# Kernel optimization log

Hardware: AMD Instinct MI355X
Metric: run time of the kernel (lower is better)

The kernel has to match this reference:

```python
import jax, jax.numpy as jnp
import numpy as np

N_NODES = 50000
N_EDGES = 800000
D_FEAT = 64


def setup_inputs() -> dict:
    key = jax.random.key(0)
    k_x, k_e, k_w = jax.random.split(key, 3)
    x = jax.random.normal(k_x, (N_NODES, D_FEAT), dtype=jnp.float32)
    edge_index = jax.random.randint(k_e, (2, N_EDGES), 0, N_NODES, dtype=jnp.int64)
    # message MLP params (phi_Theta): single linear + ReLU
    W = jax.random.normal(k_w, (D_FEAT, D_FEAT), dtype=jnp.float32) / np.sqrt(D_FEAT)
    b = jnp.zeros((D_FEAT,), dtype=jnp.float32)
    return {"x": x, "edge_index": edge_index, "W": W, "b": b}


def reference(x, edge_index, W, b):
    # flow = source_to_target: messages flow from edge_index[0] (j) to edge_index[1] (i)
    src = edge_index[0]  # j: source nodes (gather)
    dst = edge_index[1]  # i: target nodes (scatter index)
    n_nodes = x.shape[0]
    # __collect__: index_select gather of source node features -> x_j [E, D]
    x_j = x[src]
    # message: per-edge MLP  phi(x_j) = relu(x_j W + b)
    msg = jax.nn.relu(jnp.einsum('ed,df->ef', x_j, W) + b)
    # aggregate: scatter-add into target nodes (aggr='add', dim_size = size_i)
    out = jax.ops.segment_sum(msg, dst, num_segments=n_nodes)
    # update: identity
    return out
```

## Files before the change

### kernel.cpp

```cpp
#include <hip/hip_runtime.h>
#include <hip/hip_bf16.h>

#define D 64
#define CAP 64
#define EUNROLL 4

__device__ __forceinline__ float bf2f(unsigned short u) {
    return __uint_as_float((unsigned int)u << 16);
}
__device__ __forceinline__ unsigned short f2bf(float f) {
    unsigned int u = __float_as_uint(f);
    unsigned int r = (u + 0x7fffu + ((u >> 16) & 1u)) >> 16;
    return (unsigned short)r;
}

__global__ __launch_bounds__(256) void node_mlp_kernel(
    const float* __restrict__ x, const float* __restrict__ W,
    const float* __restrict__ b, unsigned short* __restrict__ m,
    int* __restrict__ cnt, int n_nodes) {
    for (int i = blockIdx.x * blockDim.x + threadIdx.x; i < n_nodes;
         i += gridDim.x * blockDim.x) cnt[i] = 0;

    const int lane = threadIdx.x & 63;
    float w[D];
    #pragma unroll
    for (int k = 0; k < D; ++k) w[k] = W[k * D + lane];
    const float bias = b[lane];

    const int wave = (blockIdx.x * blockDim.x + threadIdx.x) >> 6;
    const int nwaves = (gridDim.x * blockDim.x) >> 6;

    for (int row = wave; row < n_nodes; row += nwaves) {
        const float4* xr = (const float4*)(x + (size_t)row * D);
        float acc = bias;
        #pragma unroll
        for (int kk = 0; kk < D / 4; ++kk) {
            float4 xv = xr[kk];
            acc = fmaf(xv.x, w[4 * kk + 0], acc);
            acc = fmaf(xv.y, w[4 * kk + 1], acc);
            acc = fmaf(xv.z, w[4 * kk + 2], acc);
            acc = fmaf(xv.w, w[4 * kk + 3], acc);
        }
        m[(size_t)row * D + lane] = f2bf(fmaxf(acc, 0.0f));
    }
}

__global__ __launch_bounds__(256) void append_kernel(
    const int* __restrict__ src, const int* __restrict__ dst,
    int* __restrict__ cnt, unsigned short* __restrict__ slots, int n_edges) {
    const int base = blockIdx.x * 256 * EUNROLL + threadIdx.x;
    int s[EUNROLL], d[EUNROLL], pos[EUNROLL];
    bool ok[EUNROLL];
    #pragma unroll
    for (int i = 0; i < EUNROLL; ++i) {
        int e = base + i * 256;
        ok[i] = (e < n_edges);
        s[i] = ok[i] ? src[e] : 0;
        d[i] = ok[i] ? dst[e] : 0;
    }
    #pragma unroll
    for (int i = 0; i < EUNROLL; ++i)
        pos[i] = ok[i] ? atomicAdd(&cnt[d[i]], 1) : CAP;
    #pragma unroll
    for (int i = 0; i < EUNROLL; ++i)
        if (ok[i] && pos[i] < CAP)
            slots[(size_t)d[i] * CAP + pos[i]] = (unsigned short)s[i];
}

__global__ __launch_bounds__(256) void gather_accum_kernel(
    const unsigned short* __restrict__ slots, const int* __restrict__ cnt,
    const unsigned short* __restrict__ m, float* __restrict__ out, int n_nodes) {
    int node = blockIdx.x * 4 + (threadIdx.x >> 6);
    if (node >= n_nodes) return;
    int lane = threadIdx.x & 63;

    int c = min(cnt[node], CAP);
    unsigned int idx = (lane < c) ? (unsigned int)slots[(size_t)node * CAP + lane] : 0u;

    float acc = 0.0f;
    int k = 0;
    for (; k + 8 <= c; k += 8) {
        unsigned int s0 = __shfl(idx, k + 0);
        unsigned int s1 = __shfl(idx, k + 1);
        unsigned int s2 = __shfl(idx, k + 2);
        unsigned int s3 = __shfl(idx, k + 3);
        unsigned int s4 = __shfl(idx, k + 4);
        unsigned int s5 = __shfl(idx, k + 5);
        unsigned int s6 = __shfl(idx, k + 6);
        unsigned int s7 = __shfl(idx, k + 7);
        float v0 = bf2f(m[(size_t)s0 * D + lane]);
        float v1 = bf2f(m[(size_t)s1 * D + lane]);
        float v2 = bf2f(m[(size_t)s2 * D + lane]);
        float v3 = bf2f(m[(size_t)s3 * D + lane]);
        float v4 = bf2f(m[(size_t)s4 * D + lane]);
        float v5 = bf2f(m[(size_t)s5 * D + lane]);
        float v6 = bf2f(m[(size_t)s6 * D + lane]);
        float v7 = bf2f(m[(size_t)s7 * D + lane]);
        acc += ((v0 + v1) + (v2 + v3)) + ((v4 + v5) + (v6 + v7));
    }
    for (; k < c; ++k) {
        unsigned int s = __shfl(idx, k);
        acc += bf2f(m[(size_t)s * D + lane]);
    }
    out[(size_t)node * D + lane] = acc;
}

__global__ __launch_bounds__(256) void edge_scatter_kernel(
    const int* __restrict__ src, const int* __restrict__ dst,
    const unsigned short* __restrict__ m, float* __restrict__ out, int n_edges) {
    long long t = (long long)blockIdx.x * blockDim.x + threadIdx.x;
    int e = (int)(t >> 4);
    if (e >= n_edges) return;
    int c = (int)(t & 15) << 2;
    int s = src[e];
    int d = dst[e];
    const ushort4 v = *(const ushort4*)(m + (size_t)s * D + c);
    float* o = out + (size_t)d * D + c;
    atomicAdd(o + 0, bf2f(v.x));
    atomicAdd(o + 1, bf2f(v.y));
    atomicAdd(o + 2, bf2f(v.z));
    atomicAdd(o + 3, bf2f(v.w));
}

static inline size_t align_up(size_t v, size_t a) { return (v + a - 1) & ~(a - 1); }

extern "C" void kernel_launch(void* const* d_in, const int* in_sizes, int n_in,
                              void* d_out, int out_size, void* d_ws, size_t ws_size,
                              hipStream_t stream) {
    const float* x = (const float*)d_in[0];
    const int* edge_index = (const int*)d_in[1];
    const float* W = (const float*)d_in[2];
    const float* b = (const float*)d_in[3];
    float* out = (float*)d_out;

    const int n_nodes = in_sizes[0] / D;
    const int n_edges = in_sizes[1] / 2;
    const int* src = edge_index;
    const int* dst = edge_index + n_edges;

    size_t off = 0;
    unsigned short* m = (unsigned short*)((char*)d_ws + off);
    off = align_up(off + (size_t)n_nodes * D * sizeof(unsigned short), 256);
    int* cnt = (int*)((char*)d_ws + off);
    off = align_up(off + (size_t)n_nodes * sizeof(int), 256);
    unsigned short* slots = (unsigned short*)((char*)d_ws + off);
    off = align_up(off + (size_t)n_nodes * CAP * sizeof(unsigned short), 256);
    const size_t needed = off;

    node_mlp_kernel<<<512, 256, 0, stream>>>(x, W, b, m, cnt, n_nodes);

    if (ws_size >= needed && n_nodes <= 65536) {
        const int ablocks = (n_edges + 256 * EUNROLL - 1) / (256 * EUNROLL);
        append_kernel<<<ablocks, 256, 0, stream>>>(src, dst, cnt, slots, n_edges);
        gather_accum_kernel<<<(n_nodes + 3) / 4, 256, 0, stream>>>(
            slots, cnt, m, out, n_nodes);
    } else {
        hipMemsetAsync(d_out, 0, (size_t)out_size * sizeof(float), stream);
        long long total_threads = (long long)n_edges * 16;
        int scat_blocks = (int)((total_threads + 255) / 256);
        edge_scatter_kernel<<<scat_blocks, 256, 0, stream>>>(src, dst, m, out, n_edges);
    }
}
```

Measured before the change: 169.1 us.

## Split message table into column planes, gather in two passes with overflow list

Stores the bf16 message table as two 32-column planes so each gather pass touches a 3.2 MB table that fits better in cache. It runs two gather kernels, one per half, with two nodes per wavefront. Per-node slot capacity drops from 64 to 32, and edges beyond that go to a global overflow list that the affected nodes scan linearly. This also fixes the earlier silent dropping of edges past the cap. The cost is extra kernel launches, reading the slots and counts twice, and an O(overflow) scan for high-degree nodes.

```diff
diff --git a/kernel.cpp b/kernel.cpp
--- a/kernel.cpp
+++ b/kernel.cpp
@@ -2,8 +2,9 @@
 #include <hip/hip_bf16.h>
 
 #define D 64
-#define CAP 64
+#define CAP 32
 #define EUNROLL 4
+#define OVF_CAP 16384
 
 __device__ __forceinline__ float bf2f(unsigned short u) {
     return __uint_as_float((unsigned int)u << 16);
@@ -16,12 +17,16 @@
 
 __global__ __launch_bounds__(256) void node_mlp_kernel(
     const float* __restrict__ x, const float* __restrict__ W,
-    const float* __restrict__ b, unsigned short* __restrict__ m,
-    int* __restrict__ cnt, int n_nodes) {
+    const float* __restrict__ b, unsigned short* __restrict__ m0,
+    unsigned short* __restrict__ m1, int* __restrict__ cnt,
+    int* __restrict__ ovf_cnt, int n_nodes) {
     for (int i = blockIdx.x * blockDim.x + threadIdx.x; i < n_nodes;
          i += gridDim.x * blockDim.x) cnt[i] = 0;
+    if (blockIdx.x == 0 && threadIdx.x == 0) *ovf_cnt = 0;
 
     const int lane = threadIdx.x & 63;
+    const int l31 = lane & 31;
+    unsigned short* mp = (lane < 32) ? m0 : m1;
     float w[D];
     #pragma unroll
     for (int k = 0; k < D; ++k) w[k] = W[k * D + lane];
@@ -41,13 +46,14 @@
             acc = fmaf(xv.z, w[4 * kk + 2], acc);
             acc = fmaf(xv.w, w[4 * kk + 3], acc);
         }
-        m[(size_t)row * D + lane] = f2bf(fmaxf(acc, 0.0f));
+        mp[(size_t)row * 32 + l31] = f2bf(fmaxf(acc, 0.0f));
     }
 }
 
 __global__ __launch_bounds__(256) void append_kernel(
     const int* __restrict__ src, const int* __restrict__ dst,
-    int* __restrict__ cnt, unsigned short* __restrict__ slots, int n_edges) {
+    int* __restrict__ cnt, unsigned short* __restrict__ slots,
+    int* __restrict__ ovf_cnt, unsigned int* __restrict__ ovf, int n_edges) {
     const int base = blockIdx.x * 256 * EUNROLL + threadIdx.x;
     int s[EUNROLL], d[EUNROLL], pos[EUNROLL];
     bool ok[EUNROLL];
@@ -62,59 +68,74 @@
     for (int i = 0; i < EUNROLL; ++i)
         pos[i] = ok[i] ? atomicAdd(&cnt[d[i]], 1) : CAP;
     #pragma unroll
-    for (int i = 0; i < EUNROLL; ++i)
-        if (ok[i] && pos[i] < CAP)
+    for (int i = 0; i < EUNROLL; ++i) {
+        if (!ok[i]) continue;
+        if (pos[i] < CAP) {
             slots[(size_t)d[i] * CAP + pos[i]] = (unsigned short)s[i];
+        } else {
+            int op = atomicAdd(ovf_cnt, 1);
+            if (op < OVF_CAP)
+                ovf[op] = ((unsigned int)d[i] << 16) | (unsigned int)s[i];
+        }
+    }
 }
 
-__global__ __launch_bounds__(256) void gather_accum_kernel(
+__global__ __launch_bounds__(256) void gather_pass_kernel(
     const unsigned short* __restrict__ slots, const int* __restrict__ cnt,
-    const unsigned short* __restrict__ m, float* __restrict__ out, int n_nodes) {
-    int node = blockIdx.x * 4 + (threadIdx.x >> 6);
+    const unsigned short* __restrict__ mplane,
+    const int* __restrict__ ovf_cnt, const unsigned int* __restrict__ ovf,
+    float* __restrict__ out, int n_nodes, int col0) {
+    const int lane = threadIdx.x & 63;
+    const int l31 = lane & 31;
+    const int wave = (blockIdx.x * 256 + threadIdx.x) >> 6;
+    const int node = wave * 2 + ((lane >> 5) & 1);
     if (node >= n_nodes) return;
-    int lane = threadIdx.x & 63;
 
-    int c = min(cnt[node], CAP);
-    unsigned int idx = (lane < c) ? (unsigned int)slots[(size_t)node * CAP + lane] : 0u;
+    const int c = cnt[node];
+    const int cc = min(c, CAP);
+    unsigned int idx = (unsigned int)slots[(size_t)node * CAP + l31];
+    const int bsel = lane & 32;
 
     float acc = 0.0f;
     int k = 0;
-    for (; k + 8 <= c; k += 8) {
-        unsigned int s0 = __shfl(idx, k + 0);
-        unsigned int s1 = __shfl(idx, k + 1);
-        unsigned int s2 = __shfl(idx, k + 2);
-        unsigned int s3 = __shfl(idx, k + 3);
-        unsigned int s4 = __shfl(idx, k + 4);
-        unsigned int s5 = __shfl(idx, k + 5);
-        unsigned int s6 = __shfl(idx, k + 6);
-        unsigned int s7 = __shfl(idx, k + 7);
-        float v0 = bf2f(m[(size_t)s0 * D + lane]);
-        float v1 = bf2f(m[(size_t)s1 * D + lane]);
-        float v2 = bf2f(m[(size_t)s2 * D + lane]);
-        float v3 = bf2f(m[(size_t)s3 * D + lane]);
-        float v4 = bf2f(m[(size_t)s4 * D + lane]);
-        float v5 = bf2f(m[(size_t)s5 * D + lane]);
-        float v6 = bf2f(m[(size_t)s6 * D + lane]);
-        float v7 = bf2f(m[(size_t)s7 * D + lane]);
-        acc += ((v0 + v1) + (v2 + v3)) + ((v4 + v5) + (v6 + v7));
+    for (; k + 4 <= cc; k += 4) {
+        unsigned int s0 = __shfl(idx, bsel + k + 0);
+        unsigned int s1 = __shfl(idx, bsel + k + 1);
+        unsigned int s2 = __shfl(idx, bsel + k + 2);
+        unsigned int s3 = __shfl(idx, bsel + k + 3);
+        float v0 = bf2f(mplane[(size_t)s0 * 32 + l31]);
+        float v1 = bf2f(mplane[(size_t)s1 * 32 + l31]);
+        float v2 = bf2f(mplane[(size_t)s2 * 32 + l31]);
+        float v3 = bf2f(mplane[(size_t)s3 * 32 + l31]);
+        acc += (v0 + v1) + (v2 + v3);
     }
-    for (; k < c; ++k) {
-        unsigned int s = __shfl(idx, k);
-        acc += bf2f(m[(size_t)s * D + lane]);
+    for (; k < cc; ++k) {
+        unsigned int s = __shfl(idx, bsel + k);
+        acc += bf2f(mplane[(size_t)s * 32 + l31]);
     }
-    out[(size_t)node * D + lane] = acc;
+    if (c > CAP) {
+        int oc = min(*ovf_cnt, OVF_CAP);
+        for (int i = 0; i < oc; ++i) {
+            unsigned int e = ovf[i];
+            if ((int)(e >> 16) == node)
+                acc += bf2f(mplane[(size_t)(e & 0xFFFFu) * 32 + l31]);
+        }
+    }
+    out[(size_t)node * D + col0 + l31] = acc;
 }
 
 __global__ __launch_bounds__(256) void edge_scatter_kernel(
     const int* __restrict__ src, const int* __restrict__ dst,
-    const unsigned short* __restrict__ m, float* __restrict__ out, int n_edges) {
+    const unsigned short* __restrict__ m0, const unsigned short* __restrict__ m1,
+    float* __restrict__ out, int n_edges) {
     long long t = (long long)blockIdx.x * blockDim.x + threadIdx.x;
     int e = (int)(t >> 4);
     if (e >= n_edges) return;
     int c = (int)(t & 15) << 2;
     int s = src[e];
     int d = dst[e];
-    const ushort4 v = *(const ushort4*)(m + (size_t)s * D + c);
+    const unsigned short* mp = (c < 32) ? m0 : m1;
+    const ushort4 v = *(const ushort4*)(mp + (size_t)s * 32 + (c & 31));
     float* o = out + (size_t)d * D + c;
     atomicAdd(o + 0, bf2f(v.x));
     atomicAdd(o + 1, bf2f(v.y));
@@ -139,25 +160,36 @@
     const int* dst = edge_index + n_edges;
 
     size_t off = 0;
-    unsigned short* m = (unsigned short*)((char*)d_ws + off);
-    off = align_up(off + (size_t)n_nodes * D * sizeof(unsigned short), 256);
+    unsigned short* m0 = (unsigned short*)((char*)d_ws + off);
+    off = align_up(off + (size_t)n_nodes * 32 * sizeof(unsigned short), 256);
+    unsigned short* m1 = (unsigned short*)((char*)d_ws + off);
+    off = align_up(off + (size_t)n_nodes * 32 * sizeof(unsigned short), 256);
     int* cnt = (int*)((char*)d_ws + off);
     off = align_up(off + (size_t)n_nodes * sizeof(int), 256);
     unsigned short* slots = (unsigned short*)((char*)d_ws + off);
     off = align_up(off + (size_t)n_nodes * CAP * sizeof(unsigned short), 256);
+    int* ovf_cnt = (int*)((char*)d_ws + off);
+    off = align_up(off + sizeof(int), 256);
+    unsigned int* ovf = (unsigned int*)((char*)d_ws + off);
+    off = align_up(off + (size_t)OVF_CAP * sizeof(unsigned int), 256);
     const size_t needed = off;
 
-    node_mlp_kernel<<<512, 256, 0, stream>>>(x, W, b, m, cnt, n_nodes);
+    node_mlp_kernel<<<512, 256, 0, stream>>>(x, W, b, m0, m1, cnt, ovf_cnt, n_nodes);
 
     if (ws_size >= needed && n_nodes <= 65536) {
         const int ablocks = (n_edges + 256 * EUNROLL - 1) / (256 * EUNROLL);
-        append_kernel<<<ablocks, 256, 0, stream>>>(src, dst, cnt, slots, n_edges);
-        gather_accum_kernel<<<(n_nodes + 3) / 4, 256, 0, stream>>>(
-            slots, cnt, m, out, n_nodes);
+        append_kernel<<<ablocks, 256, 0, stream>>>(src, dst, cnt, slots,
+                                                   ovf_cnt, ovf, n_edges);
+        const int gblocks = (n_nodes + 7) / 8;
+        gather_pass_kernel<<<gblocks, 256, 0, stream>>>(
+            slots, cnt, m0, ovf_cnt, ovf, out, n_nodes, 0);
+        gather_pass_kernel<<<gblocks, 256, 0, stream>>>(
+            slots, cnt, m1, ovf_cnt, ovf, out, n_nodes, 32);
     } else {
         hipMemsetAsync(d_out, 0, (size_t)out_size * sizeof(float), stream);
         long long total_threads = (long long)n_edges * 16;
         int scat_blocks = (int)((total_threads + 255) / 256);
-        edge_scatter_kernel<<<scat_blocks, 256, 0, stream>>>(src, dst, m, out, n_edges);
+        edge_scatter_kernel<<<scat_blocks, 256, 0, stream>>>(src, dst, m0, m1,
+                                                             out, n_edges);
     }
 }
```

Measured after the change: 169.9 us. About the same (+0.5%).
